# Performance work log

Measured on AMD Instinct MI355X. Metric: run time of the kernel, lower is better.

Reference implementation:

```python
import jax, jax.numpy as jnp
import numpy as np

B, N, DIM, H, DH = 4, 2048, 1024, 16, 64
ROT = 32               # rotary dim (half of head dim)
INNER = H * DH         # 1024


def rotate_every_two(x):
    # (... (d j)) with j=2: pairs (x1, x2) -> (-x2, x1), interleaved back
    x1 = x[..., ::2]
    x2 = x[..., 1::2]
    return jnp.stack((-x2, x1), axis=-1).reshape(x.shape)


def setup_inputs() -> dict:
    key = jax.random.key(0)
    k1, k2, k3 = jax.random.split(key, 3)
    x = jax.random.normal(k1, (B, N, DIM), dtype=jnp.float32)
    # standard rotary sin/cos tables, [N, ROT], pairs share a frequency
    pos = jnp.arange(N, dtype=jnp.float32)[:, None]
    inv_freq = 1.0 / (10000.0 ** (jnp.arange(0, ROT, 2, dtype=jnp.float32) / ROT))
    ang = jnp.repeat(pos * inv_freq, 2, axis=-1)  # [N, ROT]
    sin, cos = jnp.sin(ang), jnp.cos(ang)
    Wqkv = jax.random.normal(k2, (DIM, 3 * INNER), dtype=jnp.float32) * (DIM ** -0.5)
    Wout = jax.random.normal(k3, (INNER, DIM), dtype=jnp.float32) * (INNER ** -0.5)
    return {"x": x, "sin": sin, "cos": cos, "Wqkv": Wqkv, "Wout": Wout}


def reference(x, sin, cos, Wqkv, Wout):
    scale = DH ** -0.5
    qkv = x @ Wqkv                                  # [B, N, 3*INNER]
    q, k, v = jnp.split(qkv, 3, axis=-1)

    def split_heads(t):  # 'b n (h d) -> (b h) n d'
        return t.reshape(B, N, H, DH).transpose(0, 2, 1, 3).reshape(B * H, N, DH)

    q, k, v = map(split_heads, (q, k, v))
    q = q * scale                                   # scale before RoPE (as in source)

    rd = sin.shape[-1]

    def rope(t):
        t_rot, t_pass = t[..., :rd], t[..., rd:]
        t_rot = t_rot * cos + rotate_every_two(t_rot) * sin
        return jnp.concatenate((t_rot, t_pass), axis=-1)

    q, k = rope(q), rope(k)

    sim = jnp.einsum('bid,bjd->bij', q, k)          # [(B*H), N, N]
    attn_w = jax.nn.softmax(sim, axis=-1)
    out = jnp.einsum('bij,bjd->bid', attn_w, v)     # [(B*H), N, DH]

    out = out.reshape(B, H, N, DH).transpose(0, 2, 1, 3).reshape(B, N, INNER)
    return out @ Wout                               # [B, N, DIM]
```

## Files before the change

kernel.cpp:

```cpp
#include <hip/hip_runtime.h>

typedef unsigned short u16;
typedef __attribute__((ext_vector_type(8))) short short8;
typedef __attribute__((ext_vector_type(4))) float f32x4;

#define DEV __device__ __forceinline__

DEV u16 f2bf(float f) {
  unsigned u = __float_as_uint(f);
  u += 0x7FFF + ((u >> 16) & 1);
  return (u16)(u >> 16);
}
DEV float bf2f(u16 b) { return __uint_as_float(((unsigned)b) << 16); }

DEV unsigned pk_trunc(float a, float b) {
  return __builtin_amdgcn_perm(__float_as_uint(b), __float_as_uint(a), 0x07060302u);
}

DEV void g2l16(const u16* g, u16* l) {
  __builtin_amdgcn_global_load_lds((__attribute__((address_space(1))) void*)(g),
                                   (__attribute__((address_space(3))) void*)(l), 16, 0, 0);
}

__global__ __launch_bounds__(256) void k_cvt(const float* __restrict__ x,
                                             u16* __restrict__ o, int n4) {
  int i = blockIdx.x * 256 + threadIdx.x;
  if (i >= n4) return;
  float4 v = ((const float4*)x)[i];
  ushort4 r;
  r.x = f2bf(v.x); r.y = f2bf(v.y); r.z = f2bf(v.z); r.w = f2bf(v.w);
  ((ushort4*)o)[i] = r;
}

__global__ __launch_bounds__(256) void k_tc(const float* __restrict__ W,
                                            u16* __restrict__ Wt, int K, int N) {
  __shared__ float t[32][33];
  int tx = threadIdx.x & 31, ty = threadIdx.x >> 5;
  int n0 = blockIdx.x * 32, k0 = blockIdx.y * 32;
#pragma unroll
  for (int i = 0; i < 4; ++i)
    t[ty + i * 8][tx] = W[(size_t)(k0 + ty + i * 8) * N + n0 + tx];
  __syncthreads();
#pragma unroll
  for (int i = 0; i < 4; ++i)
    Wt[(size_t)(n0 + ty + i * 8) * K + k0 + tx] = f2bf(t[tx][ty + i * 8]);
}

template <int EPI>
__global__ __launch_bounds__(256) void k_gemm(
    const u16* __restrict__ A, const u16* __restrict__ Bt,
    int M, int N, int K,
    u16* __restrict__ qw, u16* __restrict__ kw, u16* __restrict__ vw,
    float* __restrict__ of, const float* __restrict__ sn,
    const float* __restrict__ cs, float qscale) {
  __shared__ __align__(16) u16 As[128 * 64];
  __shared__ __align__(16) u16 Bs[128 * 64];
  const int t = threadIdx.x;
  const int wv = t >> 6, lane = t & 63;
  const int a15 = lane & 15, g = lane >> 4;
  const int wr = wv >> 1, wc = wv & 1;
  const int m0 = blockIdx.x * 128, n0 = blockIdx.y * 128;
  const int gr = lane >> 3, gc = (lane & 7) * 8;

  f32x4 acc[4][4];
#pragma unroll
  for (int i = 0; i < 4; ++i)
#pragma unroll
    for (int j = 0; j < 4; ++j)
#pragma unroll
      for (int r = 0; r < 4; ++r) acc[i][j][r] = 0.f;

  for (int k0 = 0; k0 < K; k0 += 64) {
#pragma unroll
    for (int c4 = 0; c4 < 4; ++c4) {
      int c = wv * 4 + c4;
      g2l16(A + (size_t)(m0 + c * 8 + gr) * K + k0 + gc, &As[c * 512]);
      g2l16(Bt + (size_t)(n0 + c * 8 + gr) * K + k0 + gc, &Bs[c * 512]);
    }
    __syncthreads();
#pragma unroll
    for (int ks = 0; ks < 2; ++ks) {
      short8 af[4], bf[4];
#pragma unroll
      for (int mi = 0; mi < 4; ++mi)
        af[mi] = *(const short8*)&As[(wr * 64 + mi * 16 + a15) * 64 + ks * 32 + g * 8];
#pragma unroll
      for (int ni = 0; ni < 4; ++ni)
        bf[ni] = *(const short8*)&Bs[(wc * 64 + ni * 16 + a15) * 64 + ks * 32 + g * 8];
#pragma unroll
      for (int mi = 0; mi < 4; ++mi)
#pragma unroll
        for (int ni = 0; ni < 4; ++ni)
          acc[mi][ni] = __builtin_amdgcn_mfma_f32_16x16x32_bf16(af[mi], bf[ni], acc[mi][ni], 0, 0, 0);
    }
    __syncthreads();
  }

  if (EPI == 0) {
    const int part = n0 >> 10;
    if (part <= 1) {
      const float sc = (part == 0) ? qscale : 1.f;
      u16* dst = (part == 0) ? qw : kw;
#pragma unroll
      for (int mi = 0; mi < 4; ++mi) {
#pragma unroll
        for (int ni = 0; ni < 4; ++ni) {
          int col = n0 + wc * 64 + ni * 16 + a15;
          int rem = col & 1023, h = rem >> 6, d = rem & 63;
          int row = m0 + wr * 64 + mi * 16 + g * 4;
          int b = row >> 11, n = row & 2047;
          size_t bh = (size_t)b * 16 + h;
#pragma unroll
          for (int r = 0; r < 4; ++r) {
            float v = acc[mi][ni][r];
            float p = __shfl_xor(v, 1);
            float outv = v;
            if (d < 32) {
              int nr = n + r;
              float c = cs[nr * 32 + d], s = sn[nr * 32 + d];
              outv = v * c + ((d & 1) ? p * s : -p * s);
            }
            dst[(bh * 2048 + n + r) * 64 + d] = f2bf(outv * sc);
          }
        }
      }
    } else {
#pragma unroll
      for (int mi = 0; mi < 4; ++mi) {
#pragma unroll
        for (int ni = 0; ni < 4; ++ni) {
          int col = n0 + wc * 64 + ni * 16 + a15;
          int rem = col & 1023, h = rem >> 6, d = rem & 63;
          int row = m0 + wr * 64 + mi * 16 + g * 4;
          int b = row >> 11, n = row & 2047;
          size_t bh = (size_t)b * 16 + h;
          ushort4 pk;
          pk.x = f2bf(acc[mi][ni][0]); pk.y = f2bf(acc[mi][ni][1]);
          pk.z = f2bf(acc[mi][ni][2]); pk.w = f2bf(acc[mi][ni][3]);
          *(ushort4*)&vw[(bh * 64 + d) * 2048 + n] = pk;
        }
      }
    }
  } else {
#pragma unroll
    for (int mi = 0; mi < 4; ++mi)
#pragma unroll
      for (int ni = 0; ni < 4; ++ni) {
        int col = n0 + wc * 64 + ni * 16 + a15;
        int row = m0 + wr * 64 + mi * 16 + g * 4;
#pragma unroll
        for (int r = 0; r < 4; ++r)
          of[(size_t)(row + r) * N + col] = acc[mi][ni][r];
      }
  }
}

__global__ __launch_bounds__(256, 3) void k_attn(
    const u16* __restrict__ q, const u16* __restrict__ kk, const u16* __restrict__ vT,
    u16* __restrict__ o) {
  __shared__ __align__(16) u16 Ks[2][4096];
  __shared__ __align__(16) u16 Vs[2][4096];
  __shared__ __align__(16) u16 Pl[4][1024];
  const int t = threadIdx.x;
  const int w = t >> 6, lane = t & 63;
  const int a15 = lane & 15, g = lane >> 4;
  const int id = blockIdx.x;
  const int bh = (id & 7) | ((id >> 7) << 3);
  const int qb = (id >> 3) & 15;
  const int q0 = qb * 128 + w * 32;
  const size_t hb = (size_t)bh * (2048 * 64);

  short8 qf[2][2];
#pragma unroll
  for (int f = 0; f < 2; ++f)
#pragma unroll
    for (int h = 0; h < 2; ++h)
      qf[f][h] = *(const short8*)&q[hb + (size_t)(q0 + f * 16 + a15) * 64 + h * 32 + g * 8];

  int ksrc[2], vsrc[2];
#pragma unroll
  for (int c = 0; c < 2; ++c) {
    int L = w * 2048 + c * 1024 + lane * 16;
    int row = L >> 7;
    int sb = L ^ ((row & 7) << 4);
    ksrc[c] = sb >> 1;
    vsrc[c] = row * 2048 + ((sb & 127) >> 1);
  }
  const u16* kg = kk + hb;
  const u16* vg = vT + (size_t)bh * (64 * 2048);

#define STAGE(b, j0) do {                                        \
    g2l16(kg + (size_t)(j0) * 64 + ksrc[0], &Ks[b][w * 1024]);   \
    g2l16(kg + (size_t)(j0) * 64 + ksrc[1], &Ks[b][w * 1024 + 512]); \
    g2l16(vg + (j0) + vsrc[0], &Vs[b][w * 1024]);                \
    g2l16(vg + (j0) + vsrc[1], &Vs[b][w * 1024 + 512]);          \
  } while (0)

  const f32x4 z4 = {0.f, 0.f, 0.f, 0.f};
  const short8 ones = {(short)0x3F80, (short)0x3F80, (short)0x3F80, (short)0x3F80,
                       (short)0x3F80, (short)0x3F80, (short)0x3F80, (short)0x3F80};
  f32x4 accO[2][4], ssum[2];
#pragma unroll
  for (int f = 0; f < 2; ++f) {
    ssum[f] = z4;
#pragma unroll
    for (int dc = 0; dc < 4; ++dc) accO[f][dc] = z4;
  }

  STAGE(0, 0);
  int cur = 0;
  for (int jt = 0; jt < 32; ++jt) {
    __syncthreads();
    if (jt < 31) STAGE(cur ^ 1, (jt + 1) * 64);

    f32x4 st[2][4];
    const char* Kb = (const char*)Ks[cur];
    __builtin_amdgcn_s_setprio(1);
#pragma unroll
    for (int jc = 0; jc < 4; ++jc) {
      int row = jc * 16 + a15;
      int sw = (row & 7) << 4;
      short8 ka0 = *(const short8*)(Kb + ((row * 128 + g * 16) ^ sw));
      short8 ka1 = *(const short8*)(Kb + ((row * 128 + 64 + g * 16) ^ sw));
      st[0][jc] = __builtin_amdgcn_mfma_f32_16x16x32_bf16(ka0, qf[0][0], z4, 0, 0, 0);
      st[0][jc] = __builtin_amdgcn_mfma_f32_16x16x32_bf16(ka1, qf[0][1], st[0][jc], 0, 0, 0);
      st[1][jc] = __builtin_amdgcn_mfma_f32_16x16x32_bf16(ka0, qf[1][0], z4, 0, 0, 0);
      st[1][jc] = __builtin_amdgcn_mfma_f32_16x16x32_bf16(ka1, qf[1][1], st[1][jc], 0, 0, 0);
    }
    __builtin_amdgcn_s_setprio(0);
    short8 vf[2][4];
    const char* Vb = (const char*)Vs[cur];
#pragma unroll
    for (int kt = 0; kt < 2; ++kt)
#pragma unroll
      for (int dc = 0; dc < 4; ++dc) {
        int row = dc * 16 + a15;
        vf[kt][dc] = *(const short8*)(Vb + ((row * 128 + kt * 64 + g * 16) ^ ((row & 7) << 4)));
      }
#pragma unroll
    for (int f = 0; f < 2; ++f) {
#pragma unroll
      for (int jc = 0; jc < 4; ++jc) {
        float e0 = __builtin_amdgcn_exp2f(st[f][jc][0]);
        float e1 = __builtin_amdgcn_exp2f(st[f][jc][1]);
        float e2 = __builtin_amdgcn_exp2f(st[f][jc][2]);
        float e3 = __builtin_amdgcn_exp2f(st[f][jc][3]);
        uint2 pw;
        pw.x = pk_trunc(e0, e1);
        pw.y = pk_trunc(e2, e3);
        int byte = (a15 * 128 + (jc * 16 + g * 4) * 2) ^ ((a15 & 7) << 4);
        *(uint2*)((char*)Pl[w] + byte) = pw;
      }
      __builtin_amdgcn_s_setprio(1);
#pragma unroll
      for (int kt = 0; kt < 2; ++kt) {
        int byteA = (a15 * 128 + kt * 64 + g * 16) ^ ((a15 & 7) << 4);
        short8 pa = *(const short8*)((const char*)Pl[w] + byteA);
        ssum[f] = __builtin_amdgcn_mfma_f32_16x16x32_bf16(pa, ones, ssum[f], 0, 0, 0);
#pragma unroll
        for (int dc = 0; dc < 4; ++dc)
          accO[f][dc] = __builtin_amdgcn_mfma_f32_16x16x32_bf16(pa, vf[kt][dc], accO[f][dc], 0, 0, 0);
      }
      __builtin_amdgcn_s_setprio(0);
    }
    cur ^= 1;
  }
#undef STAGE

  const int b = bh >> 4, h = bh & 15;
#pragma unroll
  for (int f = 0; f < 2; ++f) {
    float rs[4];
#pragma unroll
    for (int r = 0; r < 4; ++r) rs[r] = 1.f / ssum[f][r];
#pragma unroll
    for (int dc = 0; dc < 4; ++dc)
#pragma unroll
      for (int r = 0; r < 4; ++r) {
        int n = q0 + f * 16 + g * 4 + r;
        o[((size_t)b * 2048 + n) * 1024 + h * 64 + dc * 16 + a15] = f2bf(accO[f][dc][r] * rs[r]);
      }
  }
}

extern "C" void kernel_launch(void* const* d_in, const int* in_sizes, int n_in,
                              void* d_out, int out_size, void* d_ws, size_t ws_size,
                              hipStream_t stream) {
  const float* x = (const float*)d_in[0];
  const float* sn = (const float*)d_in[1];
  const float* cs = (const float*)d_in[2];
  const float* Wqkv = (const float*)d_in[3];
  const float* Wout = (const float*)d_in[4];
  float* out = (float*)d_out;

  u16* ws = (u16*)d_ws;
  u16* xb = ws;
  u16* wqkvT = xb + 8192ull * 1024;
  u16* woutT = wqkvT + 3072ull * 1024;
  u16* qw = woutT + 1024ull * 1024;
  u16* kw = qw + 64ull * 2048 * 64;
  u16* vw = kw + 64ull * 2048 * 64;
  u16* attn = xb;

  const float qscale = 0.125f * 1.4426950408889634f;

  k_cvt<<<8192, 256, 0, stream>>>(x, xb, 8192 * 1024 / 4);
  k_tc<<<dim3(96, 32), 256, 0, stream>>>(Wqkv, wqkvT, 1024, 3072);
  k_tc<<<dim3(32, 32), 256, 0, stream>>>(Wout, woutT, 1024, 1024);
  k_gemm<0><<<dim3(64, 24), 256, 0, stream>>>(xb, wqkvT, 8192, 3072, 1024,
                                              qw, kw, vw, nullptr, sn, cs, qscale);
  k_attn<<<1024, 256, 0, stream>>>(qw, kw, vw, attn);
  k_gemm<1><<<dim3(64, 8), 256, 0, stream>>>(attn, woutT, 8192, 1024, 1024,
                                             nullptr, nullptr, nullptr, out, nullptr, nullptr, 1.f);
}
```

Baseline: 217.8 us.

## Halve attention query tile per block and drop K/V double buffering

Each attention block now covers 64 query rows (16 per wave) instead of 128, so twice as many blocks are launched. K/V staging is no longer double-buffered: each tile is loaded into a single LDS buffer between two barriers, with no prefetch of the next tile. This cuts registers and LDS per block, which may raise occupancy. In exchange, each K/V tile is loaded twice as often per query, and global-load latency is now exposed on every iteration.

```diff
diff --git a/kernel.cpp b/kernel.cpp
--- a/kernel.cpp
+++ b/kernel.cpp
@@ -158,24 +158,22 @@
 __global__ __launch_bounds__(256, 3) void k_attn(
     const u16* __restrict__ q, const u16* __restrict__ kk, const u16* __restrict__ vT,
     u16* __restrict__ o) {
-  __shared__ __align__(16) u16 Ks[2][4096];
-  __shared__ __align__(16) u16 Vs[2][4096];
+  __shared__ __align__(16) u16 Ks[4096];
+  __shared__ __align__(16) u16 Vs[4096];
   __shared__ __align__(16) u16 Pl[4][1024];
   const int t = threadIdx.x;
   const int w = t >> 6, lane = t & 63;
   const int a15 = lane & 15, g = lane >> 4;
   const int id = blockIdx.x;
-  const int bh = (id & 7) | ((id >> 7) << 3);
-  const int qb = (id >> 3) & 15;
-  const int q0 = qb * 128 + w * 32;
+  const int bh = (id & 7) | ((id >> 8) << 3);
+  const int qb = (id >> 3) & 31;
+  const int q0 = qb * 64 + w * 16;
   const size_t hb = (size_t)bh * (2048 * 64);
 
-  short8 qf[2][2];
-#pragma unroll
-  for (int f = 0; f < 2; ++f)
-#pragma unroll
-    for (int h = 0; h < 2; ++h)
-      qf[f][h] = *(const short8*)&q[hb + (size_t)(q0 + f * 16 + a15) * 64 + h * 32 + g * 8];
+  short8 qf[2];
+#pragma unroll
+  for (int h = 0; h < 2; ++h)
+    qf[h] = *(const short8*)&q[hb + (size_t)(q0 + a15) * 64 + h * 32 + g * 8];
 
   int ksrc[2], vsrc[2];
 #pragma unroll
@@ -189,32 +187,28 @@
   const u16* kg = kk + hb;
   const u16* vg = vT + (size_t)bh * (64 * 2048);
 
-#define STAGE(b, j0) do {                                        \
-    g2l16(kg + (size_t)(j0) * 64 + ksrc[0], &Ks[b][w * 1024]);   \
-    g2l16(kg + (size_t)(j0) * 64 + ksrc[1], &Ks[b][w * 1024 + 512]); \
-    g2l16(vg + (j0) + vsrc[0], &Vs[b][w * 1024]);                \
-    g2l16(vg + (j0) + vsrc[1], &Vs[b][w * 1024 + 512]);          \
+#define STAGE(j0) do {                                    \
+    g2l16(kg + (size_t)(j0) * 64 + ksrc[0], &Ks[w * 1024]);      \
+    g2l16(kg + (size_t)(j0) * 64 + ksrc[1], &Ks[w * 1024 + 512]); \
+    g2l16(vg + (j0) + vsrc[0], &Vs[w * 1024]);            \
+    g2l16(vg + (j0) + vsrc[1], &Vs[w * 1024 + 512]);      \
   } while (0)
 
   const f32x4 z4 = {0.f, 0.f, 0.f, 0.f};
   const short8 ones = {(short)0x3F80, (short)0x3F80, (short)0x3F80, (short)0x3F80,
                        (short)0x3F80, (short)0x3F80, (short)0x3F80, (short)0x3F80};
-  f32x4 accO[2][4], ssum[2];
-#pragma unroll
-  for (int f = 0; f < 2; ++f) {
-    ssum[f] = z4;
-#pragma unroll
-    for (int dc = 0; dc < 4; ++dc) accO[f][dc] = z4;
-  }
-
-  STAGE(0, 0);
-  int cur = 0;
+  f32x4 accO[4], ssum = z4;
+#pragma unroll
+  for (int dc = 0; dc < 4; ++dc) accO[dc] = z4;
+
   for (int jt = 0; jt < 32; ++jt) {
+    const int j0 = jt * 64;
     __syncthreads();
-    if (jt < 31) STAGE(cur ^ 1, (jt + 1) * 64);
-
-    f32x4 st[2][4];
-    const char* Kb = (const char*)Ks[cur];
+    STAGE(j0);
+    __syncthreads();
+
+    f32x4 st[4];
+    const char* Kb = (const char*)Ks;
     __builtin_amdgcn_s_setprio(1);
 #pragma unroll
     for (int jc = 0; jc < 4; ++jc) {
@@ -222,14 +216,12 @@
       int sw = (row & 7) << 4;
       short8 ka0 = *(const short8*)(Kb + ((row * 128 + g * 16) ^ sw));
       short8 ka1 = *(const short8*)(Kb + ((row * 128 + 64 + g * 16) ^ sw));
-      st[0][jc] = __builtin_amdgcn_mfma_f32_16x16x32_bf16(ka0, qf[0][0], z4, 0, 0, 0);
-      st[0][jc] = __builtin_amdgcn_mfma_f32_16x16x32_bf16(ka1, qf[0][1], st[0][jc], 0, 0, 0);
-      st[1][jc] = __builtin_amdgcn_mfma_f32_16x16x32_bf16(ka0, qf[1][0], z4, 0, 0, 0);
-      st[1][jc] = __builtin_amdgcn_mfma_f32_16x16x32_bf16(ka1, qf[1][1], st[1][jc], 0, 0, 0);
+      st[jc] = __builtin_amdgcn_mfma_f32_16x16x32_bf16(ka0, qf[0], z4, 0, 0, 0);
+      st[jc] = __builtin_amdgcn_mfma_f32_16x16x32_bf16(ka1, qf[1], st[jc], 0, 0, 0);
     }
     __builtin_amdgcn_s_setprio(0);
     short8 vf[2][4];
-    const char* Vb = (const char*)Vs[cur];
+    const char* Vb = (const char*)Vs;
 #pragma unroll
     for (int kt = 0; kt < 2; ++kt)
 #pragma unroll
@@ -238,49 +230,42 @@
         vf[kt][dc] = *(const short8*)(Vb + ((row * 128 + kt * 64 + g * 16) ^ ((row & 7) << 4)));
       }
 #pragma unroll
-    for (int f = 0; f < 2; ++f) {
-#pragma unroll
-      for (int jc = 0; jc < 4; ++jc) {
-        float e0 = __builtin_amdgcn_exp2f(st[f][jc][0]);
-        float e1 = __builtin_amdgcn_exp2f(st[f][jc][1]);
-        float e2 = __builtin_amdgcn_exp2f(st[f][jc][2]);
-        float e3 = __builtin_amdgcn_exp2f(st[f][jc][3]);
-        uint2 pw;
-        pw.x = pk_trunc(e0, e1);
-        pw.y = pk_trunc(e2, e3);
-        int byte = (a15 * 128 + (jc * 16 + g * 4) * 2) ^ ((a15 & 7) << 4);
-        *(uint2*)((char*)Pl[w] + byte) = pw;
-      }
-      __builtin_amdgcn_s_setprio(1);
-#pragma unroll
-      for (int kt = 0; kt < 2; ++kt) {
-        int byteA = (a15 * 128 + kt * 64 + g * 16) ^ ((a15 & 7) << 4);
-        short8 pa = *(const short8*)((const char*)Pl[w] + byteA);
-        ssum[f] = __builtin_amdgcn_mfma_f32_16x16x32_bf16(pa, ones, ssum[f], 0, 0, 0);
-#pragma unroll
-        for (int dc = 0; dc < 4; ++dc)
-          accO[f][dc] = __builtin_amdgcn_mfma_f32_16x16x32_bf16(pa, vf[kt][dc], accO[f][dc], 0, 0, 0);
-      }
-      __builtin_amdgcn_s_setprio(0);
-    }
-    cur ^= 1;
+    for (int jc = 0; jc < 4; ++jc) {
+      float e0 = __builtin_amdgcn_exp2f(st[jc][0]);
+      float e1 = __builtin_amdgcn_exp2f(st[jc][1]);
+      float e2 = __builtin_amdgcn_exp2f(st[jc][2]);
+      float e3 = __builtin_amdgcn_exp2f(st[jc][3]);
+      uint2 pw;
+      pw.x = pk_trunc(e0, e1);
+      pw.y = pk_trunc(e2, e3);
+      int byte = (a15 * 128 + (jc * 16 + g * 4) * 2) ^ ((a15 & 7) << 4);
+      *(uint2*)((char*)Pl[w] + byte) = pw;
+    }
+    __builtin_amdgcn_s_setprio(1);
+#pragma unroll
+    for (int kt = 0; kt < 2; ++kt) {
+      int byteA = (a15 * 128 + kt * 64 + g * 16) ^ ((a15 & 7) << 4);
+      short8 pa = *(const short8*)((const char*)Pl[w] + byteA);
+      ssum = __builtin_amdgcn_mfma_f32_16x16x32_bf16(pa, ones, ssum, 0, 0, 0);
+#pragma unroll
+      for (int dc = 0; dc < 4; ++dc)
+        accO[dc] = __builtin_amdgcn_mfma_f32_16x16x32_bf16(pa, vf[kt][dc], accO[dc], 0, 0, 0);
+    }
+    __builtin_amdgcn_s_setprio(0);
   }
 #undef STAGE
 
   const int b = bh >> 4, h = bh & 15;
-#pragma unroll
-  for (int f = 0; f < 2; ++f) {
-    float rs[4];
-#pragma unroll
-    for (int r = 0; r < 4; ++r) rs[r] = 1.f / ssum[f][r];
-#pragma unroll
-    for (int dc = 0; dc < 4; ++dc)
-#pragma unroll
-      for (int r = 0; r < 4; ++r) {
-        int n = q0 + f * 16 + g * 4 + r;
-        o[((size_t)b * 2048 + n) * 1024 + h * 64 + dc * 16 + a15] = f2bf(accO[f][dc][r] * rs[r]);
-      }
-  }
+  float rs[4];
+#pragma unroll
+  for (int r = 0; r < 4; ++r) rs[r] = 1.f / ssum[r];
+#pragma unroll
+  for (int dc = 0; dc < 4; ++dc)
+#pragma unroll
+    for (int r = 0; r < 4; ++r) {
+      int n = q0 + g * 4 + r;
+      o[((size_t)b * 2048 + n) * 1024 + h * 64 + dc * 16 + a15] = f2bf(accO[dc][r] * rs[r]);
+    }
 }
 
 extern "C" void kernel_launch(void* const* d_in, const int* in_sizes, int n_in,
@@ -309,7 +294,7 @@
   k_tc<<<dim3(32, 32), 256, 0, stream>>>(Wout, woutT, 1024, 1024);
   k_gemm<0><<<dim3(64, 24), 256, 0, stream>>>(xb, wqkvT, 8192, 3072, 1024,
                                               qw, kw, vw, nullptr, sn, cs, qscale);
-  k_attn<<<1024, 256, 0, stream>>>(qw, kw, vw, attn);
+  k_attn<<<2048, 256, 0, stream>>>(qw, kw, vw, attn);
   k_gemm<1><<<dim3(64, 8), 256, 0, stream>>>(attn, woutT, 8192, 1024, 1024,
                                              nullptr, nullptr, nullptr, out, nullptr, nullptr, 1.f);
 }
```

Measured after the change: 222.3 us. 1.02x slower.
